# Optimization experiments

Hardware: AMD Instinct MI355X
Metric: run time of the kernel (lower is better)

## Reference

```python
import jax, jax.numpy as jnp
import numpy as np

N_NODES = 100000
N_EDGES = 1600000
IN_DIM, HID, EMB = 128, 128, 128
NUM_EDGE_FEAT = 3
BN_EPS = 1e-5


def _lin(key, fan_in, fan_out):
    k1, k2 = jax.random.split(key)
    lim = 1.0 / np.sqrt(fan_in)
    W = jax.random.uniform(k1, (fan_in, fan_out), minval=-lim, maxval=lim, dtype=jnp.float32)
    b = jax.random.uniform(k2, (fan_out,), minval=-lim, maxval=lim, dtype=jnp.float32)
    return W, b


def setup_inputs() -> dict:
    key = jax.random.key(0)
    ks = jax.random.split(key, 12)
    x = jax.random.normal(ks[0], (N_NODES, IN_DIM), dtype=jnp.float32)
    edge_index = jax.random.randint(ks[1], (2, N_EDGES), 0, N_NODES, dtype=jnp.int32)
    edge_attr = jax.random.normal(ks[2], (N_EDGES, NUM_EDGE_FEAT), dtype=jnp.float32)
    params = {}
    dims = [(IN_DIM, HID), (HID, HID), (HID, HID)]
    for i, (fi, fo) in enumerate(dims, 1):
        W, b = _lin(ks[2 + i], fi, fo)
        We, be = _lin(ks[5 + i], NUM_EDGE_FEAT, fo)
        params[f'W{i}'] = W; params[f'b{i}'] = b
        params[f'We{i}'] = We; params[f'be{i}'] = be
        params[f'g{i}'] = jnp.ones((fo,), jnp.float32)
        params[f'bt{i}'] = jnp.zeros((fo,), jnp.float32)
    Wl, bl = _lin(ks[9], HID, EMB)
    params['Wl'] = Wl; params['bl'] = bl
    return {'x': x, 'edge_index': edge_index, 'edge_attr': edge_attr, **params}


def _gcn_conv(x, row, col, edge_attr, W, b, We, be):
    h = x @ W + b                    # [N, d]
    e = edge_attr @ We + be          # [E, d]
    n = x.shape[0]
    deg = jax.ops.segment_sum(jnp.ones_like(row, dtype=h.dtype), row, num_segments=n) + 1.0
    dinv = deg ** -0.5               # deg >= 1, never inf
    norm = dinv[row] * dinv[col]     # [E]
    msg = norm[:, None] * jax.nn.relu(h[row] + e)  # gather + fused elementwise
    return jax.ops.segment_sum(msg, col, num_segments=n)  # scatter-add to targets


def _bn(x, g, bt):
    m = jnp.mean(x, axis=0)
    v = jnp.mean((x - m) ** 2, axis=0)  # biased var (training-mode batchnorm)
    return (x - m) * jax.lax.rsqrt(v + BN_EPS) * g + bt


def reference(x, edge_index, edge_attr,
              W1, b1, We1, be1, g1, bt1,
              W2, b2, We2, be2, g2, bt2,
              W3, b3, We3, be3, g3, bt3,
              Wl, bl):
    row, col = edge_index[0], edge_index[1]
    h = jax.nn.relu(_gcn_conv(x, row, col, edge_attr, W1, b1, We1, be1))
    h = _bn(h, g1, bt1)
    h = jax.nn.relu(_gcn_conv(h, row, col, edge_attr, W2, b2, We2, be2))
    h = _bn(h, g2, bt2)
    h = jax.nn.relu(_gcn_conv(h, row, col, edge_attr, W3, b3, We3, be3))
    h = _bn(h, g3, bt3)
    return h @ Wl + bl
```

## Files before the change

### kernel.cpp

```cpp
#include <hip/hip_runtime.h>
#include <stdint.h>

#define NN 100000
#define NE 1600000
#define DIM 128
#define BN_EPS 1e-5f
#define NBUCK 391
#define NBLK_GEMM 1563
#define NBLK_AGG 6250
#define NB_HIST 1024
#define CSR_PAD 32
#define NREP 64

typedef unsigned int uint;
typedef unsigned short ushort;
typedef unsigned char uchar;
typedef __attribute__((ext_vector_type(8))) short short8;
typedef __attribute__((ext_vector_type(4))) float f32x4;
typedef __attribute__((ext_vector_type(2))) float v2f;


static __device__ __forceinline__ ushort f2bf(float f) {
    uint u = __float_as_uint(f);
    u += 0x7FFF + ((u >> 16) & 1);
    return (ushort)(u >> 16);
}
static __device__ __forceinline__ float bf_lo(uint p) { return __uint_as_float(p << 16); }
static __device__ __forceinline__ float bf_hi(uint p) { return __uint_as_float(p & 0xFFFF0000u); }

static __device__ __forceinline__ v2f vfma(v2f a, v2f b, v2f c) {
    return __builtin_elementwise_fma(a, b, c);
}
static __device__ __forceinline__ v2f vbc(float s) { v2f r = {s, s}; return r; }


__global__ __launch_bounds__(256) void k_count(const int* __restrict__ ei,
                                               const float* __restrict__ x,
                                               int* __restrict__ rowCnt,
                                               int* __restrict__ colCnt,
                                               ushort* __restrict__ xb) {
    __shared__ int hr[NBUCK], hc[NBUCK];
    int tid = threadIdx.x;
    for (int b = tid; b < NBUCK; b += 256) { hr[b] = 0; hc[b] = 0; }
    __syncthreads();
    const int gstep = NB_HIST * 256;
    const int gt = blockIdx.x * 256 + tid;
    for (int e = gt; e < NE; e += gstep) {
        atomicAdd(&hr[ei[e] >> 8], 1);
        atomicAdd(&hc[ei[NE + e] >> 8], 1);
    }
    __syncthreads();
    for (int b = tid; b < NBUCK; b += 256) {
        if (hr[b]) atomicAdd(&rowCnt[b], hr[b]);
        if (hc[b]) atomicAdd(&colCnt[b], hc[b]);
    }
    for (int i = gt; i < NN * DIM / 4; i += gstep) {
        float4 v = ((const float4*)x)[i];
        ushort4 o = {f2bf(v.x), f2bf(v.y), f2bf(v.z), f2bf(v.w)};
        ((ushort4*)xb)[i] = o;
    }
}

__global__ __launch_bounds__(512) void k_scanb(const int* __restrict__ rowCnt,
                                               const int* __restrict__ colCnt,
                                               int* __restrict__ rowBase,
                                               int* __restrict__ colBase,
                                               int* __restrict__ rowCur,
                                               int* __restrict__ colCur) {
    __shared__ int s[512];
    int tid = threadIdx.x;
    int v = (tid < NBUCK) ? rowCnt[tid] : 0;
    s[tid] = v;
    __syncthreads();
    for (int d = 1; d < 512; d <<= 1) {
        int a = (tid >= d) ? s[tid - d] : 0;
        __syncthreads();
        s[tid] += a;
        __syncthreads();
    }
    if (tid < NBUCK) { int e = s[tid] - v; rowBase[tid] = e; rowCur[tid] = e; }
    if (tid == NBUCK) rowBase[NBUCK] = s[NBUCK];
    __syncthreads();
    v = (tid < NBUCK) ? colCnt[tid] : 0;
    s[tid] = v;
    __syncthreads();
    for (int d = 1; d < 512; d <<= 1) {
        int a = (tid >= d) ? s[tid - d] : 0;
        __syncthreads();
        s[tid] += a;
        __syncthreads();
    }
    if (tid < NBUCK) { int e = s[tid] - v; colBase[tid] = e; colCur[tid] = e; }
    if (tid == NBUCK) colBase[NBUCK] = s[NBUCK];
}

__global__ __launch_bounds__(256) void k_scat_row(const int* __restrict__ ei,
                                                  int* __restrict__ rowCur,
                                                  uchar* __restrict__ rowScat) {
    __shared__ int h[NBUCK], lb[NBUCK], lc[NBUCK];
    int tid = threadIdx.x;
    for (int b = tid; b < NBUCK; b += 256) { h[b] = 0; lc[b] = 0; }
    __syncthreads();
    const int gstep = NB_HIST * 256;
    const int gt = blockIdx.x * 256 + tid;
    for (int e = gt; e < NE; e += gstep) atomicAdd(&h[ei[e] >> 8], 1);
    __syncthreads();
    for (int b = tid; b < NBUCK; b += 256)
        lb[b] = h[b] ? atomicAdd(&rowCur[b], h[b]) : 0;
    __syncthreads();
    for (int e = gt; e < NE; e += gstep) {
        int r = ei[e];
        int b = r >> 8;
        int pos = lb[b] + atomicAdd(&lc[b], 1);
        rowScat[pos] = (uchar)(r & 255);
    }
}

__global__ __launch_bounds__(1024) void k_deg(const uchar* __restrict__ rowScat,
                                              const int* __restrict__ rowBase,
                                              float* __restrict__ dinv) {
    __shared__ int h[256];
    int tid = threadIdx.x;
    int b = blockIdx.x;
    if (tid < 256) h[tid] = 0;
    __syncthreads();
    int base = rowBase[b], cnt = rowBase[b + 1] - base;
    for (int i = tid; i < cnt; i += 1024) atomicAdd(&h[rowScat[base + i]], 1);
    __syncthreads();
    if (tid < 256) {
        int node = b * 256 + tid;
        if (node < NN) dinv[node] = rsqrtf((float)h[tid] + 1.0f);
    }
}

__global__ __launch_bounds__(256) void k_scat_col(const int* __restrict__ ei,
                                                  const float* __restrict__ ea,
                                                  const float* __restrict__ dinv,
                                                  int* __restrict__ colCur,
                                                  uint4* __restrict__ tmp) {
    __shared__ int h[NBUCK], lb[NBUCK], lc[NBUCK];
    int tid = threadIdx.x;
    for (int b = tid; b < NBUCK; b += 256) { h[b] = 0; lc[b] = 0; }
    __syncthreads();
    const int gstep = NB_HIST * 256;
    const int gt = blockIdx.x * 256 + tid;
    for (int e = gt; e < NE; e += gstep) atomicAdd(&h[ei[NE + e] >> 8], 1);
    __syncthreads();
    for (int b = tid; b < NBUCK; b += 256)
        lb[b] = h[b] ? atomicAdd(&colCur[b], h[b]) : 0;
    __syncthreads();
    for (int e = gt; e < NE; e += gstep) {
        int r = ei[e];
        int c = ei[NE + e];
        int b = c >> 8;
        int pos = lb[b] + atomicAdd(&lc[b], 1);
        uint4 rec;
        rec.x = __float_as_uint(dinv[r] * dinv[c]);
        rec.y = ((uint)f2bf(ea[e * 3]) << 16) | (uint)f2bf(ea[e * 3 + 1]);
        rec.z = ((uint)f2bf(ea[e * 3 + 2]) << 16) | (uint)(c & 255);
        rec.w = (uint)r;
        tmp[pos] = rec;
    }
}

__global__ __launch_bounds__(1024) void k_sort_col(const uint4* __restrict__ tmp,
                                                   const int* __restrict__ colBase,
                                                   uint4* __restrict__ csr,
                                                   int* __restrict__ offs) {
    __shared__ int hh[256], sc[256], cur[256];
    int tid = threadIdx.x;
    int b = blockIdx.x;
    if (tid < 256) hh[tid] = 0;
    __syncthreads();
    int base = colBase[b], cnt = colBase[b + 1] - base;
    for (int i = tid; i < cnt; i += 1024) atomicAdd(&hh[tmp[base + i].z & 255], 1);
    __syncthreads();
    int v = 0;
    if (tid < 256) { v = hh[tid]; sc[tid] = v; }
    __syncthreads();
    for (int d = 1; d < 256; d <<= 1) {
        int add = 0;
        if (tid < 256 && tid >= d) add = sc[tid - d];
        __syncthreads();
        if (tid < 256) sc[tid] += add;
        __syncthreads();
    }
    if (tid < 256) {
        int excl = sc[tid] - v;
        int node = b * 256 + tid;
        if (node < NN) offs[node] = base + excl;
        if (b == NBUCK - 1 && tid == 0) offs[NN] = NE;
        cur[tid] = excl;
    }
    __syncthreads();
    for (int i = tid; i < cnt; i += 1024) {
        uint4 rec = tmp[base + i];
        int f = rec.z & 255;
        int pos = atomicAdd(&cur[f], 1);
        csr[base + pos] = rec;
    }
}


__global__ __launch_bounds__(128) void k_prep(const float* __restrict__ W,
                                              const float* __restrict__ b,
                                              const float* __restrict__ g,
                                              const float* __restrict__ bt,
                                              const float* __restrict__ sprev,
                                              float* __restrict__ snext,
                                              int mode,
                                              ushort* __restrict__ Wt,
                                              float* __restrict__ beff) {
    __shared__ float s[DIM];
    int k = threadIdx.x;
    if (k < 64) snext[blockIdx.x * 64 + k] = 0.0f;
    float A = 1.0f, B = 0.0f;
    if (mode) {
        float sm = 0.0f, sq = 0.0f;
        for (int r = 0; r < NREP; ++r) {
            sm += sprev[r * 256 + k];
            sq += sprev[r * 256 + 128 + k];
        }
        float m = sm * (1.0f / NN);
        float var = sq * (1.0f / NN) - m * m;
        float rs = rsqrtf(var + BN_EPS);
        A = rs * g[k];
        B = bt[k] - m * A;
    }
    if (blockIdx.x < DIM) {
        int n = blockIdx.x;
        Wt[n * DIM + k] = f2bf(A * W[k * DIM + n]);
    } else {
        int j = blockIdx.x - DIM;
        s[k] = B * W[k * DIM + j];
        __syncthreads();
        for (int d = 64; d > 0; d >>= 1) {
            if (k < d) s[k] += s[k + d];
            __syncthreads();
        }
        if (k == 0) beff[j] = b[j] + s[0];
    }
}


#define GEMM_MFMA_BODY(Abf, Wt)                                                     \
    const int lane = threadIdx.x & 63;                                              \
    const int wv   = threadIdx.x >> 6;                                              \
    const int m    = lane & 15;                                                     \
    const int quad = lane >> 4;                                                     \
    const int row0 = blockIdx.x * 64 + wv * 16;                                     \
    const int rr   = min(row0 + m, NN - 1);                                         \
    const short8* ap = (const short8*)&Abf[(size_t)rr * DIM + quad * 8];            \
    short8 a0 = ap[0];                                                              \
    short8 a1 = ap[4];                                                              \
    short8 a2 = ap[8];                                                              \
    short8 a3 = ap[12];                                                             \
    f32x4 acc[8];                                                                   \
    _Pragma("unroll")                                                               \
    for (int nt = 0; nt < 8; ++nt) {                                                \
        const short8* bp = (const short8*)&Wt[(size_t)(nt * 16 + m) * DIM + quad * 8]; \
        f32x4 c = {0.f, 0.f, 0.f, 0.f};                                             \
        c = __builtin_amdgcn_mfma_f32_16x16x32_bf16(a0, bp[0],  c, 0, 0, 0);        \
        c = __builtin_amdgcn_mfma_f32_16x16x32_bf16(a1, bp[4],  c, 0, 0, 0);        \
        c = __builtin_amdgcn_mfma_f32_16x16x32_bf16(a2, bp[8],  c, 0, 0, 0);        \
        c = __builtin_amdgcn_mfma_f32_16x16x32_bf16(a3, bp[12], c, 0, 0, 0);        \
        acc[nt] = c;                                                                \
    }                                                                               \
    const int rbase = row0 + quad * 4;

__global__ __launch_bounds__(256) void k_gemm_mf_bf(const ushort* __restrict__ Abf,
                                                    const ushort* __restrict__ Wt,
                                                    const float* __restrict__ beff,
                                                    ushort* __restrict__ Y) {
    GEMM_MFMA_BODY(Abf, Wt)
#pragma unroll
    for (int nt = 0; nt < 8; ++nt) {
        int col = nt * 16 + m;
        float bb = beff[col];
#pragma unroll
        for (int i = 0; i < 4; ++i) {
            int row = rbase + i;
            if (row < NN) Y[(size_t)row * DIM + col] = f2bf(acc[nt][i] + bb);
        }
    }
}

__global__ __launch_bounds__(256) void k_gemm_mf_f32(const ushort* __restrict__ Abf,
                                                     const ushort* __restrict__ Wt,
                                                     const float* __restrict__ beff,
                                                     float* __restrict__ Y) {
    GEMM_MFMA_BODY(Abf, Wt)
#pragma unroll
    for (int nt = 0; nt < 8; ++nt) {
        int col = nt * 16 + m;
        float bb = beff[col];
#pragma unroll
        for (int i = 0; i < 4; ++i) {
            int row = rbase + i;
            if (row < NN) Y[(size_t)row * DIM + col] = acc[nt][i] + bb;
        }
    }
}


static __device__ __forceinline__ void edge_compute(float4 r, float4 hv, float n,
                                                    const v2f* __restrict__ w0,
                                                    const v2f* __restrict__ w1,
                                                    const v2f* __restrict__ w2,
                                                    const v2f* __restrict__ vbe,
                                                    v2f* __restrict__ acc) {
    uint py = __float_as_uint(r.y), pz = __float_as_uint(r.z);
    v2f va0 = vbc(bf_hi(py)), va1 = vbc(bf_lo(py)), va2 = vbc(bf_hi(pz));
    v2f vn = vbc(n);
    uint hx = __float_as_uint(hv.x), hy = __float_as_uint(hv.y);
    uint hz = __float_as_uint(hv.z), hw = __float_as_uint(hv.w);
    v2f hp[4] = {{bf_lo(hx), bf_hi(hx)}, {bf_lo(hy), bf_hi(hy)},
                 {bf_lo(hz), bf_hi(hz)}, {bf_lo(hw), bf_hi(hw)}};
    const v2f z = {0.0f, 0.0f};
#pragma unroll
    for (int j = 0; j < 4; ++j) {
        v2f e = vfma(va2, w2[j], vbe[j]);
        e = vfma(va1, w1[j], e);
        e = vfma(va0, w0[j], e);
        v2f u = hp[j] + e;
        u = __builtin_elementwise_max(u, z);
        acc[j] = vfma(vn, u, acc[j]);
    }
}

__global__ __launch_bounds__(256) void k_agg(const float4* __restrict__ h4,
                                             const float4* __restrict__ csr,
                                             const int* __restrict__ offs,
                                             const float* __restrict__ We,
                                             const float* __restrict__ be,
                                             uint* __restrict__ tb,
                                             float* __restrict__ stats) {
    __shared__ float pbuf[4][256];
    int wv = threadIdx.x >> 6;
    int lane = threadIdx.x & 63;
    int q  = lane >> 4;
    int oc = lane & 15;
    int j0 = oc * 8;

    float4 t0, t1;
    t0 = *(const float4*)&We[j0];             t1 = *(const float4*)&We[j0 + 4];
    v2f w0[4] = {{t0.x, t0.y}, {t0.z, t0.w}, {t1.x, t1.y}, {t1.z, t1.w}};
    t0 = *(const float4*)&We[DIM + j0];       t1 = *(const float4*)&We[DIM + j0 + 4];
    v2f w1[4] = {{t0.x, t0.y}, {t0.z, t0.w}, {t1.x, t1.y}, {t1.z, t1.w}};
    t0 = *(const float4*)&We[2 * DIM + j0];   t1 = *(const float4*)&We[2 * DIM + j0 + 4];
    v2f w2[4] = {{t0.x, t0.y}, {t0.z, t0.w}, {t1.x, t1.y}, {t1.z, t1.w}};
    t0 = *(const float4*)&be[j0];             t1 = *(const float4*)&be[j0 + 4];
    v2f vbe[4] = {{t0.x, t0.y}, {t0.z, t0.w}, {t1.x, t1.y}, {t1.z, t1.w}};

    v2f smv[4] = {{0,0},{0,0},{0,0},{0,0}};
    v2f sqv[4] = {{0,0},{0,0},{0,0},{0,0}};

    const int v0 = blockIdx.x * 16 + wv * 4;
    int ofs[5];
#pragma unroll
    for (int k = 0; k < 5; ++k) ofs[k] = offs[v0 + k];

    for (int it = 0; it < 4; ++it) {
        int v = v0 + it;
        v2f acc[4] = {{0,0},{0,0},{0,0},{0,0}};
        int s0 = ofs[it], e0 = ofs[it + 1];

        float4 rA1 = csr[s0 + q];
        float4 rA2 = csr[s0 + 4 + q];
        float4 rB1 = csr[s0 + 8 + q];
        float4 rB2 = csr[s0 + 12 + q];
        float4 hA1 = h4[(size_t)__float_as_int(rA1.w) * 16 + oc];
        float4 hA2 = h4[(size_t)__float_as_int(rA2.w) * 16 + oc];

#pragma unroll 2
        for (int base = s0; base < e0; base += 8) {
            float4 hB1 = h4[(size_t)__float_as_int(rB1.w) * 16 + oc];
            float4 hB2 = h4[(size_t)__float_as_int(rB2.w) * 16 + oc];
            float4 rC1 = csr[base + 16 + q];
            float4 rC2 = csr[base + 20 + q];
            float n1 = (base + q < e0) ? rA1.x : 0.0f;
            float n2 = (base + 4 + q < e0) ? rA2.x : 0.0f;
            edge_compute(rA1, hA1, n1, w0, w1, w2, vbe, acc);
            edge_compute(rA2, hA2, n2, w0, w1, w2, vbe, acc);
            rA1 = rB1; rA2 = rB2; rB1 = rC1; rB2 = rC2;
            hA1 = hB1; hA2 = hB2;
        }

#pragma unroll
        for (int j = 0; j < 4; ++j) {
            acc[j].x += __shfl_xor(acc[j].x, 16); acc[j].x += __shfl_xor(acc[j].x, 32);
            acc[j].y += __shfl_xor(acc[j].y, 16); acc[j].y += __shfl_xor(acc[j].y, 32);
        }

        if (q == 0) {
            uint4 pk;
            uint pw[4];
#pragma unroll
            for (int j = 0; j < 4; ++j) {
                acc[j].x = fmaxf(acc[j].x, 0.0f);
                acc[j].y = fmaxf(acc[j].y, 0.0f);
                smv[j] = smv[j] + acc[j];
                sqv[j] = vfma(acc[j], acc[j], sqv[j]);
                pw[j] = ((uint)f2bf(acc[j].y) << 16) | f2bf(acc[j].x);
            }
            pk.x = pw[0]; pk.y = pw[1]; pk.z = pw[2]; pk.w = pw[3];
            *(uint4*)&tb[(size_t)v * 64 + oc * 4] = pk;
        }
    }

    if (q == 0) {
#pragma unroll
        for (int j = 0; j < 4; ++j) {
            pbuf[wv][j0 + 2 * j]       = smv[j].x;
            pbuf[wv][j0 + 2 * j + 1]   = smv[j].y;
            pbuf[wv][128 + j0 + 2 * j]     = sqv[j].x;
            pbuf[wv][128 + j0 + 2 * j + 1] = sqv[j].y;
        }
    }
    __syncthreads();
    int tid = threadIdx.x;
    float s = pbuf[0][tid] + pbuf[1][tid] + pbuf[2][tid] + pbuf[3][tid];
    atomicAdd(&stats[(blockIdx.x & (NREP - 1)) * 256 + tid], s);
}


static inline char* alignp(char* p, size_t a) {
    return (char*)(((uintptr_t)p + a - 1) & ~(uintptr_t)(a - 1));
}

extern "C" void kernel_launch(void* const* d_in, const int* in_sizes, int n_in,
                              void* d_out, int out_size, void* d_ws, size_t ws_size,
                              hipStream_t stream) {
    const float* x   = (const float*)d_in[0];
    const int*   ei  = (const int*)d_in[1];
    const float* ea  = (const float*)d_in[2];
    const float* Wp[3]  = {(const float*)d_in[3],  (const float*)d_in[9],  (const float*)d_in[15]};
    const float* bp[3]  = {(const float*)d_in[4],  (const float*)d_in[10], (const float*)d_in[16]};
    const float* Wep[3] = {(const float*)d_in[5],  (const float*)d_in[11], (const float*)d_in[17]};
    const float* bep[3] = {(const float*)d_in[6],  (const float*)d_in[12], (const float*)d_in[18]};
    const float* gp[3]  = {(const float*)d_in[7],  (const float*)d_in[13], (const float*)d_in[19]};
    const float* btp[3] = {(const float*)d_in[8],  (const float*)d_in[14], (const float*)d_in[20]};
    const float* Wl  = (const float*)d_in[21];
    const float* bl  = (const float*)d_in[22];
    float* out = (float*)d_out;

    char* p = (char*)d_ws;
    auto alloc = [&](size_t bytes) -> void* {
        p = alignp(p, 256);
        void* r = (void*)p;
        p += bytes;
        return r;
    };

    int*    bcnt     = (int*)alloc(2 * NBUCK * sizeof(int));
    int*    rowCnt   = bcnt;
    int*    colCnt   = bcnt + NBUCK;
    int*    rowBase  = (int*)alloc((NBUCK + 1) * sizeof(int));
    int*    colBase  = (int*)alloc((NBUCK + 1) * sizeof(int));
    int*    rowCur   = (int*)alloc(NBUCK * sizeof(int));
    int*    colCur   = (int*)alloc(NBUCK * sizeof(int));
    int*    offs     = (int*)alloc((NN + 1) * sizeof(int));
    float*  dinv     = (float*)alloc(NN * sizeof(float));
    uchar*  rowScat  = (uchar*)alloc(NE * sizeof(uchar));
    uint4*  csr      = (uint4*)alloc(((size_t)NE + CSR_PAD) * sizeof(uint4));
    ushort* x_bf     = (ushort*)alloc((size_t)NN * DIM * sizeof(ushort));
    ushort* h_bf     = (ushort*)alloc((size_t)NN * DIM * sizeof(ushort));
    ushort* t_bf     = (ushort*)alloc((size_t)NN * DIM * sizeof(ushort));
    ushort* Wt       = (ushort*)alloc(DIM * DIM * sizeof(ushort));
    float*  beff     = (float*)alloc(DIM * sizeof(float));
    float*  sb0      = (float*)alloc((size_t)NREP * 256 * sizeof(float));
    float*  sb1      = (float*)alloc((size_t)NREP * 256 * sizeof(float));

    uint4* tmp = (uint4*)t_bf;

    hipMemsetAsync(bcnt, 0, 2 * NBUCK * sizeof(int), stream);
    hipMemsetAsync(csr + NE, 0, CSR_PAD * sizeof(uint4), stream);
    k_count<<<NB_HIST, 256, 0, stream>>>(ei, x, rowCnt, colCnt, x_bf);
    k_scanb<<<1, 512, 0, stream>>>(rowCnt, colCnt, rowBase, colBase, rowCur, colCur);
    k_scat_row<<<NB_HIST, 256, 0, stream>>>(ei, rowCur, rowScat);
    k_deg<<<NBUCK, 1024, 0, stream>>>(rowScat, rowBase, dinv);
    k_scat_col<<<NB_HIST, 256, 0, stream>>>(ei, ea, dinv, colCur, tmp);
    k_sort_col<<<NBUCK, 1024, 0, stream>>>(tmp, colBase, csr, offs);

    float* sbs[2] = {sb0, sb1};
    const ushort* Xbf = x_bf;
    for (int l = 0; l < 3; ++l) {
        float* scur = sbs[l & 1];
        float* sprev = sbs[(l + 1) & 1];
        const float* gg = (l == 0) ? gp[0] : gp[l - 1];
        const float* bb = (l == 0) ? btp[0] : btp[l - 1];
        k_prep<<<256, 128, 0, stream>>>(Wp[l], bp[l], gg, bb, sprev, scur,
                                        (l == 0) ? 0 : 1, Wt, beff);
        k_gemm_mf_bf<<<NBLK_GEMM, 256, 0, stream>>>(Xbf, Wt, beff, h_bf);
        k_agg<<<NBLK_AGG, 256, 0, stream>>>((const float4*)h_bf, (const float4*)csr, offs,
                                            Wep[l], bep[l], (uint*)t_bf, scur);
        Xbf = t_bf;
    }

    k_prep<<<256, 128, 0, stream>>>(Wl, bl, gp[2], btp[2], sb0, sb1, 1, Wt, beff);
    k_gemm_mf_f32<<<NBLK_GEMM, 256, 0, stream>>>(t_bf, Wt, beff, out);
}
```

Measured before the change: 747.2 us.

## Build CSR with per-node global atomics instead of two-level bucket sort

Replaces the bucketed two-pass counting sort (bucket histograms, row scatter, degree kernel, column scatter to temp, per-bucket local sort) with direct per-node degree counting via global atomics, a three-stage prefix scan over node in-degrees, and a single scatter pass that places each edge record at offs[c] plus an atomic cursor. This removes several full passes over edge data and the temporary buffer. In exchange it adds 3.2M global atomics on random addresses and nondeterministic edge order within each node's list, which changes float summation order in aggregation.

```diff
diff --git a/kernel.cpp b/kernel.cpp
--- a/kernel.cpp
+++ b/kernel.cpp
@@ -36,23 +36,14 @@
 
 __global__ __launch_bounds__(256) void k_count(const int* __restrict__ ei,
                                                const float* __restrict__ x,
-                                               int* __restrict__ rowCnt,
-                                               int* __restrict__ colCnt,
+                                               int* __restrict__ deg,
+                                               int* __restrict__ indeg,
                                                ushort* __restrict__ xb) {
-    __shared__ int hr[NBUCK], hc[NBUCK];
-    int tid = threadIdx.x;
-    for (int b = tid; b < NBUCK; b += 256) { hr[b] = 0; hc[b] = 0; }
-    __syncthreads();
     const int gstep = NB_HIST * 256;
-    const int gt = blockIdx.x * 256 + tid;
+    const int gt = blockIdx.x * 256 + threadIdx.x;
     for (int e = gt; e < NE; e += gstep) {
-        atomicAdd(&hr[ei[e] >> 8], 1);
-        atomicAdd(&hc[ei[NE + e] >> 8], 1);
-    }
-    __syncthreads();
-    for (int b = tid; b < NBUCK; b += 256) {
-        if (hr[b]) atomicAdd(&rowCnt[b], hr[b]);
-        if (hc[b]) atomicAdd(&colCnt[b], hc[b]);
+        atomicAdd(&deg[ei[e]], 1);
+        atomicAdd(&indeg[ei[NE + e]], 1);
     }
     for (int i = gt; i < NN * DIM / 4; i += gstep) {
         float4 v = ((const float4*)x)[i];
@@ -61,15 +52,30 @@
     }
 }
 
-__global__ __launch_bounds__(512) void k_scanb(const int* __restrict__ rowCnt,
-                                               const int* __restrict__ colCnt,
-                                               int* __restrict__ rowBase,
-                                               int* __restrict__ colBase,
-                                               int* __restrict__ rowCur,
-                                               int* __restrict__ colCur) {
+__global__ __launch_bounds__(256) void k_scanA(const int* __restrict__ indeg,
+                                               int* __restrict__ offs,
+                                               int* __restrict__ blockSum) {
+    __shared__ int s[256];
+    int tid = threadIdx.x, b = blockIdx.x;
+    int node = b * 256 + tid;
+    int v = (node < NN) ? indeg[node] : 0;
+    s[tid] = v;
+    __syncthreads();
+    for (int d = 1; d < 256; d <<= 1) {
+        int a = (tid >= d) ? s[tid - d] : 0;
+        __syncthreads();
+        s[tid] += a;
+        __syncthreads();
+    }
+    if (node < NN) offs[node] = s[tid] - v;
+    if (tid == 255) blockSum[b] = s[255];
+}
+
+__global__ __launch_bounds__(512) void k_scanB(const int* __restrict__ blockSum,
+                                               int* __restrict__ blockBase) {
     __shared__ int s[512];
     int tid = threadIdx.x;
-    int v = (tid < NBUCK) ? rowCnt[tid] : 0;
+    int v = (tid < NBUCK) ? blockSum[tid] : 0;
     s[tid] = v;
     __syncthreads();
     for (int d = 1; d < 512; d <<= 1) {
@@ -78,126 +84,42 @@
         s[tid] += a;
         __syncthreads();
     }
-    if (tid < NBUCK) { int e = s[tid] - v; rowBase[tid] = e; rowCur[tid] = e; }
-    if (tid == NBUCK) rowBase[NBUCK] = s[NBUCK];
-    __syncthreads();
-    v = (tid < NBUCK) ? colCnt[tid] : 0;
-    s[tid] = v;
-    __syncthreads();
-    for (int d = 1; d < 512; d <<= 1) {
-        int a = (tid >= d) ? s[tid - d] : 0;
-        __syncthreads();
-        s[tid] += a;
-        __syncthreads();
-    }
-    if (tid < NBUCK) { int e = s[tid] - v; colBase[tid] = e; colCur[tid] = e; }
-    if (tid == NBUCK) colBase[NBUCK] = s[NBUCK];
-}
-
-__global__ __launch_bounds__(256) void k_scat_row(const int* __restrict__ ei,
-                                                  int* __restrict__ rowCur,
-                                                  uchar* __restrict__ rowScat) {
-    __shared__ int h[NBUCK], lb[NBUCK], lc[NBUCK];
-    int tid = threadIdx.x;
-    for (int b = tid; b < NBUCK; b += 256) { h[b] = 0; lc[b] = 0; }
-    __syncthreads();
+    if (tid < NBUCK) blockBase[tid] = s[tid] - v;
+}
+
+__global__ __launch_bounds__(256) void k_scanC(const int* __restrict__ deg,
+                                               const int* __restrict__ blockBase,
+                                               int* __restrict__ offs,
+                                               int* __restrict__ cur,
+                                               float* __restrict__ dinv) {
+    int b = blockIdx.x, tid = threadIdx.x;
+    int node = b * 256 + tid;
+    if (node < NN) {
+        offs[node] += blockBase[b];
+        cur[node] = 0;
+        dinv[node] = rsqrtf((float)deg[node] + 1.0f);
+    }
+    if (b == NBUCK - 1 && tid == 0) offs[NN] = NE;
+}
+
+__global__ __launch_bounds__(256) void k_scat(const int* __restrict__ ei,
+                                              const float* __restrict__ ea,
+                                              const float* __restrict__ dinv,
+                                              const int* __restrict__ offs,
+                                              int* __restrict__ cur,
+                                              uint4* __restrict__ csr) {
     const int gstep = NB_HIST * 256;
-    const int gt = blockIdx.x * 256 + tid;
-    for (int e = gt; e < NE; e += gstep) atomicAdd(&h[ei[e] >> 8], 1);
-    __syncthreads();
-    for (int b = tid; b < NBUCK; b += 256)
-        lb[b] = h[b] ? atomicAdd(&rowCur[b], h[b]) : 0;
-    __syncthreads();
-    for (int e = gt; e < NE; e += gstep) {
-        int r = ei[e];
-        int b = r >> 8;
-        int pos = lb[b] + atomicAdd(&lc[b], 1);
-        rowScat[pos] = (uchar)(r & 255);
-    }
-}
-
-__global__ __launch_bounds__(1024) void k_deg(const uchar* __restrict__ rowScat,
-                                              const int* __restrict__ rowBase,
-                                              float* __restrict__ dinv) {
-    __shared__ int h[256];
-    int tid = threadIdx.x;
-    int b = blockIdx.x;
-    if (tid < 256) h[tid] = 0;
-    __syncthreads();
-    int base = rowBase[b], cnt = rowBase[b + 1] - base;
-    for (int i = tid; i < cnt; i += 1024) atomicAdd(&h[rowScat[base + i]], 1);
-    __syncthreads();
-    if (tid < 256) {
-        int node = b * 256 + tid;
-        if (node < NN) dinv[node] = rsqrtf((float)h[tid] + 1.0f);
-    }
-}
-
-__global__ __launch_bounds__(256) void k_scat_col(const int* __restrict__ ei,
-                                                  const float* __restrict__ ea,
-                                                  const float* __restrict__ dinv,
-                                                  int* __restrict__ colCur,
-                                                  uint4* __restrict__ tmp) {
-    __shared__ int h[NBUCK], lb[NBUCK], lc[NBUCK];
-    int tid = threadIdx.x;
-    for (int b = tid; b < NBUCK; b += 256) { h[b] = 0; lc[b] = 0; }
-    __syncthreads();
-    const int gstep = NB_HIST * 256;
-    const int gt = blockIdx.x * 256 + tid;
-    for (int e = gt; e < NE; e += gstep) atomicAdd(&h[ei[NE + e] >> 8], 1);
-    __syncthreads();
-    for (int b = tid; b < NBUCK; b += 256)
-        lb[b] = h[b] ? atomicAdd(&colCur[b], h[b]) : 0;
-    __syncthreads();
+    const int gt = blockIdx.x * 256 + threadIdx.x;
     for (int e = gt; e < NE; e += gstep) {
         int r = ei[e];
         int c = ei[NE + e];
-        int b = c >> 8;
-        int pos = lb[b] + atomicAdd(&lc[b], 1);
         uint4 rec;
         rec.x = __float_as_uint(dinv[r] * dinv[c]);
         rec.y = ((uint)f2bf(ea[e * 3]) << 16) | (uint)f2bf(ea[e * 3 + 1]);
-        rec.z = ((uint)f2bf(ea[e * 3 + 2]) << 16) | (uint)(c & 255);
+        rec.z = ((uint)f2bf(ea[e * 3 + 2]) << 16);
         rec.w = (uint)r;
-        tmp[pos] = rec;
-    }
-}
-
-__global__ __launch_bounds__(1024) void k_sort_col(const uint4* __restrict__ tmp,
-                                                   const int* __restrict__ colBase,
-                                                   uint4* __restrict__ csr,
-                                                   int* __restrict__ offs) {
-    __shared__ int hh[256], sc[256], cur[256];
-    int tid = threadIdx.x;
-    int b = blockIdx.x;
-    if (tid < 256) hh[tid] = 0;
-    __syncthreads();
-    int base = colBase[b], cnt = colBase[b + 1] - base;
-    for (int i = tid; i < cnt; i += 1024) atomicAdd(&hh[tmp[base + i].z & 255], 1);
-    __syncthreads();
-    int v = 0;
-    if (tid < 256) { v = hh[tid]; sc[tid] = v; }
-    __syncthreads();
-    for (int d = 1; d < 256; d <<= 1) {
-        int add = 0;
-        if (tid < 256 && tid >= d) add = sc[tid - d];
-        __syncthreads();
-        if (tid < 256) sc[tid] += add;
-        __syncthreads();
-    }
-    if (tid < 256) {
-        int excl = sc[tid] - v;
-        int node = b * 256 + tid;
-        if (node < NN) offs[node] = base + excl;
-        if (b == NBUCK - 1 && tid == 0) offs[NN] = NE;
-        cur[tid] = excl;
-    }
-    __syncthreads();
-    for (int i = tid; i < cnt; i += 1024) {
-        uint4 rec = tmp[base + i];
-        int f = rec.z & 255;
-        int pos = atomicAdd(&cur[f], 1);
-        csr[base + pos] = rec;
+        int pos = offs[c] + atomicAdd(&cur[c], 1);
+        csr[pos] = rec;
     }
 }
 
@@ -452,16 +374,14 @@
         return r;
     };
 
-    int*    bcnt     = (int*)alloc(2 * NBUCK * sizeof(int));
-    int*    rowCnt   = bcnt;
-    int*    colCnt   = bcnt + NBUCK;
-    int*    rowBase  = (int*)alloc((NBUCK + 1) * sizeof(int));
-    int*    colBase  = (int*)alloc((NBUCK + 1) * sizeof(int));
-    int*    rowCur   = (int*)alloc(NBUCK * sizeof(int));
-    int*    colCur   = (int*)alloc(NBUCK * sizeof(int));
+    int*    degs     = (int*)alloc(2 * NN * sizeof(int));
+    int*    deg      = degs;
+    int*    indeg    = degs + NN;
+    int*    cur      = (int*)alloc(NN * sizeof(int));
+    int*    blockSum = (int*)alloc(NBUCK * sizeof(int));
+    int*    blockBase= (int*)alloc(NBUCK * sizeof(int));
     int*    offs     = (int*)alloc((NN + 1) * sizeof(int));
     float*  dinv     = (float*)alloc(NN * sizeof(float));
-    uchar*  rowScat  = (uchar*)alloc(NE * sizeof(uchar));
     uint4*  csr      = (uint4*)alloc(((size_t)NE + CSR_PAD) * sizeof(uint4));
     ushort* x_bf     = (ushort*)alloc((size_t)NN * DIM * sizeof(ushort));
     ushort* h_bf     = (ushort*)alloc((size_t)NN * DIM * sizeof(ushort));
@@ -471,16 +391,13 @@
     float*  sb0      = (float*)alloc((size_t)NREP * 256 * sizeof(float));
     float*  sb1      = (float*)alloc((size_t)NREP * 256 * sizeof(float));
 
-    uint4* tmp = (uint4*)t_bf;
-
-    hipMemsetAsync(bcnt, 0, 2 * NBUCK * sizeof(int), stream);
+    hipMemsetAsync(degs, 0, 2 * NN * sizeof(int), stream);
     hipMemsetAsync(csr + NE, 0, CSR_PAD * sizeof(uint4), stream);
-    k_count<<<NB_HIST, 256, 0, stream>>>(ei, x, rowCnt, colCnt, x_bf);
-    k_scanb<<<1, 512, 0, stream>>>(rowCnt, colCnt, rowBase, colBase, rowCur, colCur);
-    k_scat_row<<<NB_HIST, 256, 0, stream>>>(ei, rowCur, rowScat);
-    k_deg<<<NBUCK, 1024, 0, stream>>>(rowScat, rowBase, dinv);
-    k_scat_col<<<NB_HIST, 256, 0, stream>>>(ei, ea, dinv, colCur, tmp);
-    k_sort_col<<<NBUCK, 1024, 0, stream>>>(tmp, colBase, csr, offs);
+    k_count<<<NB_HIST, 256, 0, stream>>>(ei, x, deg, indeg, x_bf);
+    k_scanA<<<NBUCK, 256, 0, stream>>>(indeg, offs, blockSum);
+    k_scanB<<<1, 512, 0, stream>>>(blockSum, blockBase);
+    k_scanC<<<NBUCK, 256, 0, stream>>>(deg, blockBase, offs, cur, dinv);
+    k_scat<<<NB_HIST, 256, 0, stream>>>(ei, ea, dinv, offs, cur, csr);
 
     float* sbs[2] = {sb0, sb1};
     const ushort* Xbf = x_bf;
```

New measurement: 803.1 us. 7.5% more time.

## Fuse row/col scatter passes, move norm into sort, convert x inside first GEMM

Applied to the files above, without the earlier changes.

Merges the separate row and column bucket-scatter kernels into one pass over the edge list and moves the dinv[r]*dinv[c] norm computation into the per-bucket sort kernel, using a shared-memory copy of the target dinv. Drops the standalone float-to-bf16 conversion of x and has the first-layer GEMM read fp32 x and convert it in registers. Also halves the histogram grid size. This removes one kernel launch and one full pass over edge indices, plus a write and re-read of x in bf16. In exchange the first GEMM reads twice as many bytes, and the sort kernel now does a random gather of dinv per edge.

```diff
diff --git a/kernel.cpp b/kernel.cpp
--- a/kernel.cpp
+++ b/kernel.cpp
@@ -8,7 +8,7 @@
 #define NBUCK 391
 #define NBLK_GEMM 1563
 #define NBLK_AGG 6250
-#define NB_HIST 1024
+#define NB_HIST 512
 #define CSR_PAD 32
 #define NREP 64
 
@@ -35,10 +35,8 @@
 
 
 __global__ __launch_bounds__(256) void k_count(const int* __restrict__ ei,
-                                               const float* __restrict__ x,
                                                int* __restrict__ rowCnt,
-                                               int* __restrict__ colCnt,
-                                               ushort* __restrict__ xb) {
+                                               int* __restrict__ colCnt) {
     __shared__ int hr[NBUCK], hc[NBUCK];
     int tid = threadIdx.x;
     for (int b = tid; b < NBUCK; b += 256) { hr[b] = 0; hc[b] = 0; }
@@ -53,11 +51,6 @@
     for (int b = tid; b < NBUCK; b += 256) {
         if (hr[b]) atomicAdd(&rowCnt[b], hr[b]);
         if (hc[b]) atomicAdd(&colCnt[b], hc[b]);
-    }
-    for (int i = gt; i < NN * DIM / 4; i += gstep) {
-        float4 v = ((const float4*)x)[i];
-        ushort4 o = {f2bf(v.x), f2bf(v.y), f2bf(v.z), f2bf(v.w)};
-        ((ushort4*)xb)[i] = o;
     }
 }
 
@@ -94,25 +87,40 @@
     if (tid == NBUCK) colBase[NBUCK] = s[NBUCK];
 }
 
-__global__ __launch_bounds__(256) void k_scat_row(const int* __restrict__ ei,
-                                                  int* __restrict__ rowCur,
-                                                  uchar* __restrict__ rowScat) {
-    __shared__ int h[NBUCK], lb[NBUCK], lc[NBUCK];
+__global__ __launch_bounds__(256) void k_scat(const int* __restrict__ ei,
+                                              const float* __restrict__ ea,
+                                              int* __restrict__ rowCur,
+                                              int* __restrict__ colCur,
+                                              uchar* __restrict__ rowScat,
+                                              uint4* __restrict__ tmp) {
+    __shared__ int hr[NBUCK], hc[NBUCK], lbr[NBUCK], lbc[NBUCK], lcr[NBUCK], lcc[NBUCK];
     int tid = threadIdx.x;
-    for (int b = tid; b < NBUCK; b += 256) { h[b] = 0; lc[b] = 0; }
+    for (int b = tid; b < NBUCK; b += 256) { hr[b] = 0; hc[b] = 0; lcr[b] = 0; lcc[b] = 0; }
     __syncthreads();
     const int gstep = NB_HIST * 256;
     const int gt = blockIdx.x * 256 + tid;
-    for (int e = gt; e < NE; e += gstep) atomicAdd(&h[ei[e] >> 8], 1);
-    __syncthreads();
-    for (int b = tid; b < NBUCK; b += 256)
-        lb[b] = h[b] ? atomicAdd(&rowCur[b], h[b]) : 0;
+    for (int e = gt; e < NE; e += gstep) {
+        atomicAdd(&hr[ei[e] >> 8], 1);
+        atomicAdd(&hc[ei[NE + e] >> 8], 1);
+    }
+    __syncthreads();
+    for (int b = tid; b < NBUCK; b += 256) {
+        lbr[b] = hr[b] ? atomicAdd(&rowCur[b], hr[b]) : 0;
+        lbc[b] = hc[b] ? atomicAdd(&colCur[b], hc[b]) : 0;
+    }
     __syncthreads();
     for (int e = gt; e < NE; e += gstep) {
         int r = ei[e];
-        int b = r >> 8;
-        int pos = lb[b] + atomicAdd(&lc[b], 1);
-        rowScat[pos] = (uchar)(r & 255);
+        int c = ei[NE + e];
+        int posr = lbr[r >> 8] + atomicAdd(&lcr[r >> 8], 1);
+        rowScat[posr] = (uchar)(r & 255);
+        uint4 rec;
+        rec.x = 0u;
+        rec.y = ((uint)f2bf(ea[e * 3]) << 16) | (uint)f2bf(ea[e * 3 + 1]);
+        rec.z = ((uint)f2bf(ea[e * 3 + 2]) << 16) | (uint)(c & 255);
+        rec.w = (uint)r;
+        int posc = lbc[c >> 8] + atomicAdd(&lcc[c >> 8], 1);
+        tmp[posc] = rec;
     }
 }
 
@@ -133,44 +141,20 @@
     }
 }
 
-__global__ __launch_bounds__(256) void k_scat_col(const int* __restrict__ ei,
-                                                  const float* __restrict__ ea,
-                                                  const float* __restrict__ dinv,
-                                                  int* __restrict__ colCur,
-                                                  uint4* __restrict__ tmp) {
-    __shared__ int h[NBUCK], lb[NBUCK], lc[NBUCK];
-    int tid = threadIdx.x;
-    for (int b = tid; b < NBUCK; b += 256) { h[b] = 0; lc[b] = 0; }
-    __syncthreads();
-    const int gstep = NB_HIST * 256;
-    const int gt = blockIdx.x * 256 + tid;
-    for (int e = gt; e < NE; e += gstep) atomicAdd(&h[ei[NE + e] >> 8], 1);
-    __syncthreads();
-    for (int b = tid; b < NBUCK; b += 256)
-        lb[b] = h[b] ? atomicAdd(&colCur[b], h[b]) : 0;
-    __syncthreads();
-    for (int e = gt; e < NE; e += gstep) {
-        int r = ei[e];
-        int c = ei[NE + e];
-        int b = c >> 8;
-        int pos = lb[b] + atomicAdd(&lc[b], 1);
-        uint4 rec;
-        rec.x = __float_as_uint(dinv[r] * dinv[c]);
-        rec.y = ((uint)f2bf(ea[e * 3]) << 16) | (uint)f2bf(ea[e * 3 + 1]);
-        rec.z = ((uint)f2bf(ea[e * 3 + 2]) << 16) | (uint)(c & 255);
-        rec.w = (uint)r;
-        tmp[pos] = rec;
-    }
-}
-
 __global__ __launch_bounds__(1024) void k_sort_col(const uint4* __restrict__ tmp,
                                                    const int* __restrict__ colBase,
+                                                   const float* __restrict__ dinv,
                                                    uint4* __restrict__ csr,
                                                    int* __restrict__ offs) {
     __shared__ int hh[256], sc[256], cur[256];
+    __shared__ float dloc[256];
     int tid = threadIdx.x;
     int b = blockIdx.x;
-    if (tid < 256) hh[tid] = 0;
+    if (tid < 256) {
+        hh[tid] = 0;
+        int node = b * 256 + tid;
+        dloc[tid] = (node < NN) ? dinv[node] : 0.0f;
+    }
     __syncthreads();
     int base = colBase[b], cnt = colBase[b + 1] - base;
     for (int i = tid; i < cnt; i += 1024) atomicAdd(&hh[tmp[base + i].z & 255], 1);
@@ -196,6 +180,7 @@
     for (int i = tid; i < cnt; i += 1024) {
         uint4 rec = tmp[base + i];
         int f = rec.z & 255;
+        rec.x = __float_as_uint(dinv[(int)rec.w] * dloc[f]);
         int pos = atomicAdd(&cur[f], 1);
         csr[base + pos] = rec;
     }
@@ -243,18 +228,7 @@
 }
 
 
-#define GEMM_MFMA_BODY(Abf, Wt)                                                     \
-    const int lane = threadIdx.x & 63;                                              \
-    const int wv   = threadIdx.x >> 6;                                              \
-    const int m    = lane & 15;                                                     \
-    const int quad = lane >> 4;                                                     \
-    const int row0 = blockIdx.x * 64 + wv * 16;                                     \
-    const int rr   = min(row0 + m, NN - 1);                                         \
-    const short8* ap = (const short8*)&Abf[(size_t)rr * DIM + quad * 8];            \
-    short8 a0 = ap[0];                                                              \
-    short8 a1 = ap[4];                                                              \
-    short8 a2 = ap[8];                                                              \
-    short8 a3 = ap[12];                                                             \
+#define GEMM_MFMA_CORE(a0, a1, a2, a3, Wt)                                          \
     f32x4 acc[8];                                                                   \
     _Pragma("unroll")                                                               \
     for (int nt = 0; nt < 8; ++nt) {                                                \
@@ -268,11 +242,57 @@
     }                                                                               \
     const int rbase = row0 + quad * 4;
 
+#define GEMM_LANE_SETUP                                                             \
+    const int lane = threadIdx.x & 63;                                              \
+    const int wv   = threadIdx.x >> 6;                                              \
+    const int m    = lane & 15;                                                     \
+    const int quad = lane >> 4;                                                     \
+    const int row0 = blockIdx.x * 64 + wv * 16;                                     \
+    const int rr   = min(row0 + m, NN - 1);
+
+static __device__ __forceinline__ short8 cvt8(float4 a, float4 b) {
+    short8 r;
+    r[0] = (short)f2bf(a.x); r[1] = (short)f2bf(a.y);
+    r[2] = (short)f2bf(a.z); r[3] = (short)f2bf(a.w);
+    r[4] = (short)f2bf(b.x); r[5] = (short)f2bf(b.y);
+    r[6] = (short)f2bf(b.z); r[7] = (short)f2bf(b.w);
+    return r;
+}
+
+__global__ __launch_bounds__(256) void k_gemm_mf_f32in(const float* __restrict__ Af,
+                                                       const ushort* __restrict__ Wt,
+                                                       const float* __restrict__ beff,
+                                                       ushort* __restrict__ Y) {
+    GEMM_LANE_SETUP
+    const float4* apf = (const float4*)&Af[(size_t)rr * DIM] + quad * 2;
+    short8 a0 = cvt8(apf[0],  apf[1]);
+    short8 a1 = cvt8(apf[8],  apf[9]);
+    short8 a2 = cvt8(apf[16], apf[17]);
+    short8 a3 = cvt8(apf[24], apf[25]);
+    GEMM_MFMA_CORE(a0, a1, a2, a3, Wt)
+#pragma unroll
+    for (int nt = 0; nt < 8; ++nt) {
+        int col = nt * 16 + m;
+        float bb = beff[col];
+#pragma unroll
+        for (int i = 0; i < 4; ++i) {
+            int row = rbase + i;
+            if (row < NN) Y[(size_t)row * DIM + col] = f2bf(acc[nt][i] + bb);
+        }
+    }
+}
+
 __global__ __launch_bounds__(256) void k_gemm_mf_bf(const ushort* __restrict__ Abf,
                                                     const ushort* __restrict__ Wt,
                                                     const float* __restrict__ beff,
                                                     ushort* __restrict__ Y) {
-    GEMM_MFMA_BODY(Abf, Wt)
+    GEMM_LANE_SETUP
+    const short8* ap = (const short8*)&Abf[(size_t)rr * DIM + quad * 8];
+    short8 a0 = ap[0];
+    short8 a1 = ap[4];
+    short8 a2 = ap[8];
+    short8 a3 = ap[12];
+    GEMM_MFMA_CORE(a0, a1, a2, a3, Wt)
 #pragma unroll
     for (int nt = 0; nt < 8; ++nt) {
         int col = nt * 16 + m;
@@ -289,7 +309,13 @@
                                                      const ushort* __restrict__ Wt,
                                                      const float* __restrict__ beff,
                                                      float* __restrict__ Y) {
-    GEMM_MFMA_BODY(Abf, Wt)
+    GEMM_LANE_SETUP
+    const short8* ap = (const short8*)&Abf[(size_t)rr * DIM + quad * 8];
+    short8 a0 = ap[0];
+    short8 a1 = ap[4];
+    short8 a2 = ap[8];
+    short8 a3 = ap[12];
+    GEMM_MFMA_CORE(a0, a1, a2, a3, Wt)
 #pragma unroll
     for (int nt = 0; nt < 8; ++nt) {
         int col = nt * 16 + m;
@@ -463,7 +489,6 @@
     float*  dinv     = (float*)alloc(NN * sizeof(float));
     uchar*  rowScat  = (uchar*)alloc(NE * sizeof(uchar));
     uint4*  csr      = (uint4*)alloc(((size_t)NE + CSR_PAD) * sizeof(uint4));
-    ushort* x_bf     = (ushort*)alloc((size_t)NN * DIM * sizeof(ushort));
     ushort* h_bf     = (ushort*)alloc((size_t)NN * DIM * sizeof(ushort));
     ushort* t_bf     = (ushort*)alloc((size_t)NN * DIM * sizeof(ushort));
     ushort* Wt       = (ushort*)alloc(DIM * DIM * sizeof(ushort));
@@ -475,15 +500,13 @@
 
     hipMemsetAsync(bcnt, 0, 2 * NBUCK * sizeof(int), stream);
     hipMemsetAsync(csr + NE, 0, CSR_PAD * sizeof(uint4), stream);
-    k_count<<<NB_HIST, 256, 0, stream>>>(ei, x, rowCnt, colCnt, x_bf);
+    k_count<<<NB_HIST, 256, 0, stream>>>(ei, rowCnt, colCnt);
     k_scanb<<<1, 512, 0, stream>>>(rowCnt, colCnt, rowBase, colBase, rowCur, colCur);
-    k_scat_row<<<NB_HIST, 256, 0, stream>>>(ei, rowCur, rowScat);
+    k_scat<<<NB_HIST, 256, 0, stream>>>(ei, ea, rowCur, colCur, rowScat, tmp);
     k_deg<<<NBUCK, 1024, 0, stream>>>(rowScat, rowBase, dinv);
-    k_scat_col<<<NB_HIST, 256, 0, stream>>>(ei, ea, dinv, colCur, tmp);
-    k_sort_col<<<NBUCK, 1024, 0, stream>>>(tmp, colBase, csr, offs);
+    k_sort_col<<<NBUCK, 1024, 0, stream>>>(tmp, colBase, dinv, csr, offs);
 
     float* sbs[2] = {sb0, sb1};
-    const ushort* Xbf = x_bf;
     for (int l = 0; l < 3; ++l) {
         float* scur = sbs[l & 1];
         float* sprev = sbs[(l + 1) & 1];
@@ -491,10 +514,12 @@
         const float* bb = (l == 0) ? btp[0] : btp[l - 1];
         k_prep<<<256, 128, 0, stream>>>(Wp[l], bp[l], gg, bb, sprev, scur,
                                         (l == 0) ? 0 : 1, Wt, beff);
-        k_gemm_mf_bf<<<NBLK_GEMM, 256, 0, stream>>>(Xbf, Wt, beff, h_bf);
+        if (l == 0)
+            k_gemm_mf_f32in<<<NBLK_GEMM, 256, 0, stream>>>(x, Wt, beff, h_bf);
+        else
+            k_gemm_mf_bf<<<NBLK_GEMM, 256, 0, stream>>>(t_bf, Wt, beff, h_bf);
         k_agg<<<NBLK_AGG, 256, 0, stream>>>((const float4*)h_bf, (const float4*)csr, offs,
                                             Wep[l], bep[l], (uint*)t_bf, scur);
-        Xbf = t_bf;
     }
 
     k_prep<<<256, 128, 0, stream>>>(Wl, bl, gp[2], btp[2], sb0, sb1, 1, Wt, beff);
```

New measurement: 694.6 us. 7.0% less time.
